# Performance work log

Measured on AMD Instinct MI355X. Metric: run time of the kernel, lower is better.

The kernel has to match this reference:

```python
import jax, jax.numpy as jnp
import numpy as np

D_IN = 1024
D_OUT = 1024


def setup_inputs() -> dict:
    key = jax.random.key(0)
    kx, kq, kk, kv = jax.random.split(key, 4)
    B, S = 4, 2048
    scale = 1.0 / np.sqrt(D_IN)
    return {
        "x": jax.random.normal(kx, (B, S, D_IN), dtype=jnp.float32),
        "Wq": jax.random.normal(kq, (D_IN, D_OUT), dtype=jnp.float32) * scale,
        "Wk": jax.random.normal(kk, (D_IN, D_OUT), dtype=jnp.float32) * scale,
        "Wv": jax.random.normal(kv, (D_IN, D_OUT), dtype=jnp.float32) * scale,
    }


def reference(x, Wq, Wk, Wv):
    # x: [B, S, D_in]; single-head causal attention (dropout=0 -> identity)
    q = jnp.einsum("bsd,de->bse", x, Wq)
    k = jnp.einsum("bsd,de->bse", x, Wk)
    v = jnp.einsum("bsd,de->bse", x, Wv)
    S = x.shape[1]
    d_k = k.shape[-1]
    scores = jnp.einsum("bqe,bke->bqk", q, k) / jnp.sqrt(jnp.float32(d_k))
    causal = jnp.tril(jnp.ones((S, S), dtype=bool))  # True = keep
    scores = jnp.where(causal, scores, -jnp.inf)
    weights = jax.nn.softmax(scores, axis=-1)
    return jnp.einsum("bqk,bke->bqe", weights, v)
```

## Files before the change

### kernel.cpp

```cpp
#include <hip/hip_runtime.h>

typedef unsigned short u16;
typedef __bf16 bf16x8_v __attribute__((ext_vector_type(8)));
typedef float f32x4 __attribute__((ext_vector_type(4)));

__device__ __forceinline__ u16 f2bf(float f) {
    unsigned u = __float_as_uint(f);
    unsigned r = u + 0x7fffu + ((u >> 16) & 1u);
    return (u16)(r >> 16);
}
__device__ __forceinline__ float bf2f(u16 h) {
    return __uint_as_float(((unsigned)h) << 16);
}

__device__ __forceinline__ void gll16(const u16* g, u16* l) {
    __builtin_amdgcn_global_load_lds(
        (const __attribute__((address_space(1))) void*)g,
        (__attribute__((address_space(3))) void*)l, 16, 0, 0);
}

#define EXP_SHIFT 12.0f

__device__ __forceinline__ float* srow_ptr(u16* Sb, int b, int i) {
    return (float*)((char*)Sb + (size_t)b * 8388608 +
                    ((i >> 9) << 12) + 2048 + ((size_t)(i & 511) << 2));
}

__global__ __launch_bounds__(256) void k_prep(const float* __restrict__ x,
                                              const float* __restrict__ Wq,
                                              const float* __restrict__ Wk,
                                              const float* __restrict__ Wv,
                                              u16* __restrict__ xb,
                                              u16* __restrict__ Wt3,
                                              u16* __restrict__ Sb,
                                              float* __restrict__ O) {
    __shared__ float tile[32][33];
    const int bid = blockIdx.x, tid = threadIdx.x;
    if (bid < 4096) {
        int i = (bid * 256 + tid) * 8;
        float4 a = *(const float4*)(x + i);
        float4 bb = *(const float4*)(x + i + 4);
        union { int4 p; u16 h[8]; } o;
        o.h[0] = f2bf(a.x);  o.h[1] = f2bf(a.y);  o.h[2] = f2bf(a.z);  o.h[3] = f2bf(a.w);
        o.h[4] = f2bf(bb.x); o.h[5] = f2bf(bb.y); o.h[6] = f2bf(bb.z); o.h[7] = f2bf(bb.w);
        *(int4*)(xb + i) = o.p;
    } else if (bid < 7168) {
        const int w = bid - 4096;
        const int z = w >> 10, rem = w & 1023;
        const int bx = rem & 31, by = rem >> 5;
        const float* W = (z == 0) ? Wq : (z == 1) ? Wk : Wv;
        u16* Wt = Wt3 + (size_t)z * 1024 * 1024;
        const int tx = tid & 31, ty = tid >> 5;
#pragma unroll
        for (int r = 0; r < 4; ++r)
            tile[ty + r * 8][tx] = W[(by * 32 + ty + r * 8) * 1024 + bx * 32 + tx];
        __syncthreads();
#pragma unroll
        for (int r = 0; r < 4; ++r)
            Wt[(bx * 32 + ty + r * 8) * 1024 + by * 32 + tx] =
                f2bf(tile[tx][ty + r * 8]);
    } else if (bid == 7168) {
        const int chunk = tid >> 7;
        const int t = tid & 127;
        int4 z4 = {0, 0, 0, 0};
#pragma unroll
        for (int c = 0; c < 8; ++c) {
            const int cc = c * 2 + chunk;
            char* p = (char*)Sb + (size_t)(cc >> 2) * 8388608 +
                      ((cc & 3) << 12) + 2048;
            *(int4*)(p + t * 16) = z4;
        }
    } else {
        float4* O4 = (float4*)O;
        const size_t base = (size_t)(bid - 7169) * 1024 + tid;
        float4 z4 = {0.f, 0.f, 0.f, 0.f};
        O4[base] = z4; O4[base + 256] = z4;
        O4[base + 512] = z4; O4[base + 768] = z4;
    }
}

__device__ __forceinline__ void gemm_core_nt(const u16* __restrict__ A,
                                             const u16* __restrict__ B,
                                             int lda, int ldb, int kLen,
                                             u16* smem, f32x4 acc[4][4]) {
    u16* As = smem;
    u16* Bs = smem + 128 * 64;
    const int tid = threadIdx.x;
    const int wave = tid >> 6;
    const int lane = tid & 63;
    const int rowA = tid >> 3;
    const int kcs  = (tid & 7) ^ (rowA & 7);
    const int row16 = lane & 15;
    const int quad = lane >> 4;
    const int sw = row16 & 7;
    const int wm = (wave >> 1) * 64;
    const int wn = (wave & 1) * 64;

#pragma unroll
    for (int i = 0; i < 4; ++i)
#pragma unroll
        for (int j = 0; j < 4; ++j) {
            f32x4 z = {0.f, 0.f, 0.f, 0.f};
            acc[i][j] = z;
        }

    const u16* Ag[4]; const u16* Bg[4];
    u16 *AsB[4], *BsB[4];
#pragma unroll
    for (int u = 0; u < 4; ++u) {
        Ag[u] = A + (size_t)(u * 32 + rowA) * lda + kcs * 8;
        Bg[u] = B + (size_t)(u * 32 + rowA) * ldb + kcs * 8;
        AsB[u] = As + (u * 256 + wave * 64) * 8;
        BsB[u] = Bs + (u * 256 + wave * 64) * 8;
    }

    const int ktiles = kLen >> 6;
    for (int kt = 0; kt < ktiles; ++kt) {
        __syncthreads();
#pragma unroll
        for (int u = 0; u < 4; ++u) gll16(Ag[u] + kt * 64, AsB[u]);
#pragma unroll
        for (int u = 0; u < 4; ++u) gll16(Bg[u] + kt * 64, BsB[u]);
        __syncthreads();
#pragma unroll
        for (int h = 0; h < 2; ++h) {
            bf16x8_v af[4], bfv[4];
            const int cp = (h * 4 + quad);
#pragma unroll
            for (int i = 0; i < 4; ++i)
                af[i] = *(const bf16x8_v*)(As + (wm + i * 16 + row16) * 64 +
                                           (cp ^ sw) * 8);
#pragma unroll
            for (int j = 0; j < 4; ++j)
                bfv[j] = *(const bf16x8_v*)(Bs + (wn + j * 16 + row16) * 64 +
                                            (cp ^ sw) * 8);
#pragma unroll
            for (int i = 0; i < 4; ++i)
#pragma unroll
                for (int j = 0; j < 4; ++j)
                    acc[i][j] = __builtin_amdgcn_mfma_f32_16x16x32_bf16(
                        af[i], bfv[j], acc[i][j], 0, 0, 0);
        }
    }
}

__device__ __forceinline__ void epi_bf16(const f32x4 acc[4][4], u16* smem,
                                         u16* __restrict__ g, int ldg) {
    const int tid = threadIdx.x;
    const int wave = tid >> 6, lane = tid & 63;
    const int row16 = lane & 15, quad = lane >> 4;
    u16* Ts = smem + wave * 2048;
#pragma unroll
    for (int jh = 0; jh < 2; ++jh) {
#pragma unroll
        for (int i = 0; i < 4; ++i)
#pragma unroll
            for (int jj = 0; jj < 2; ++jj) {
                const int j = jh * 2 + jj;
#pragma unroll
                for (int r = 0; r < 4; ++r)
                    Ts[(i * 16 + quad * 4 + r) * 32 + jj * 16 + row16] =
                        f2bf(acc[i][j][r]);
            }
#pragma unroll
        for (int s = 0; s < 4; ++s) {
            const int row = s * 16 + (lane >> 2);
            int4 val = *(const int4*)(Ts + row * 32 + (lane & 3) * 8);
            *(int4*)(g + (size_t)row * ldg + jh * 32 + (lane & 3) * 8) = val;
        }
    }
}

__device__ __forceinline__ void epi_vt(const f32x4 acc[4][4], u16* smem,
                                       u16* __restrict__ Vt, int m0w, int n0w) {
    const int tid = threadIdx.x;
    const int wave = tid >> 6, lane = tid & 63;
    const int row16 = lane & 15, quad = lane >> 4;
    const int b = m0w >> 11;
    const int sBase = m0w & 2047;
    u16* Ts = smem + wave * 4608;
#pragma unroll
    for (int p = 0; p < 2; ++p) {
#pragma unroll
        for (int i = 0; i < 4; ++i)
#pragma unroll
            for (int jj = 0; jj < 2; ++jj) {
                const int j = p * 2 + jj;
                union { unsigned long long d; u16 h[4]; } o;
#pragma unroll
                for (int r = 0; r < 4; ++r) o.h[r] = f2bf(acc[i][j][r]);
                *(unsigned long long*)(Ts + (jj * 16 + row16) * 72 +
                                       i * 16 + quad * 4) = o.d;
            }
#pragma unroll
        for (int rr = 0; rr < 4; ++rr) {
            const int ln = rr * 8 + (lane >> 3);
            const int ck = lane & 7;
            int4 val = *(const int4*)(Ts + ln * 72 + ck * 8);
            const int n = n0w + p * 32 + ln;
            *(int4*)(Vt + ((size_t)b * 1024 + n) * 2048 + sBase + ck * 8) = val;
        }
    }
}

__global__ __launch_bounds__(256, 3) void k_projqk(const u16* __restrict__ X,
                                                   const u16* __restrict__ Wt3,
                                                   u16* __restrict__ Qb,
                                                   u16* __restrict__ Kb) {
    __shared__ u16 smem[16384];
    const int n0g = blockIdx.x * 128, m0 = blockIdx.y * 128;
    f32x4 acc[4][4];
    gemm_core_nt(X + (size_t)m0 * 1024, Wt3 + (size_t)n0g * 1024, 1024, 1024, 1024,
                 smem, acc);
    const int tid = threadIdx.x, wave = tid >> 6;
    const int wm = (wave >> 1) * 64, wn = (wave & 1) * 64;
    __syncthreads();
    u16* Y = (n0g < 1024) ? Qb : Kb;
    const int n0 = n0g & 1023;
    epi_bf16(acc, smem, Y + (size_t)(m0 + wm) * 1024 + n0 + wn, 1024);
}

__global__ __launch_bounds__(256, 3) void k_mix(const u16* __restrict__ X,
                                                const u16* __restrict__ Wt3,
                                                u16* __restrict__ Vt,
                                                const u16* __restrict__ Q,
                                                const u16* __restrict__ Kb,
                                                u16* __restrict__ Sb) {
    __shared__ u16 smem[18432];
    const int bid = blockIdx.x, tid = threadIdx.x;
    const int wave = tid >> 6, lane = tid & 63;
    const int wm = (wave >> 1) * 64, wn = (wave & 1) * 64;
    const int row16 = lane & 15, quad = lane >> 4;

    if (bid < 512) {
        const int nv = bid & 7, m0 = (bid >> 3) * 128;
        f32x4 acc[4][4];
        gemm_core_nt(X + (size_t)m0 * 1024,
                     Wt3 + (size_t)(2048 + nv * 128) * 1024, 1024, 1024, 1024,
                     smem, acc);
        __syncthreads();
        epi_vt(acc, smem, Vt, m0 + wm, nv * 128 + wn);
        return;
    }
    const int lin = bid - 512;
    const int lin2 = (lin & 7) * 68 + (lin >> 3);
    int t = lin2 % 136, b = lin2 / 136;
    int mt = 0;
    while ((mt + 1) * (mt + 2) / 2 <= t) ++mt;
    int nt = t - mt * (mt + 1) / 2;
    const u16* Qp = Q + (size_t)b * 2048 * 1024 + (size_t)mt * 128 * 1024;
    const u16* Kp = Kb + (size_t)b * 2048 * 1024 + (size_t)nt * 128 * 1024;
    u16* Sp = Sb + (size_t)b * 2048 * 2048;
    f32x4 acc[4][4];
    gemm_core_nt(Qp, Kp, 1024, 1024, 1024, smem, acc);
    const int mBase = mt * 128 + wm;
    const int nBase = nt * 128 + wn;
    u16* Ts = smem + wave * 2048;
    float rs[4][4];
#pragma unroll
    for (int i = 0; i < 4; ++i)
#pragma unroll
        for (int r = 0; r < 4; ++r) rs[i][r] = 0.f;

    __syncthreads();
#pragma unroll
    for (int jh = 0; jh < 2; ++jh) {
#pragma unroll
        for (int i = 0; i < 4; ++i)
#pragma unroll
            for (int jj = 0; jj < 2; ++jj) {
                const int j = jh * 2 + jj;
                const int n = nBase + jh * 32 + jj * 16 + row16;
#pragma unroll
                for (int r = 0; r < 4; ++r) {
                    const int m = mBase + i * 16 + quad * 4 + r;
                    float e = 0.f;
                    if (n <= m)
                        e = __expf(acc[i][j][r] * 0.03125f - EXP_SHIFT);
                    rs[i][r] += e;
                    Ts[(i * 16 + quad * 4 + r) * 32 + jj * 16 + row16] = f2bf(e);
                }
            }
#pragma unroll
        for (int s = 0; s < 4; ++s) {
            const int row = s * 16 + (lane >> 2);
            int4 val = *(const int4*)(Ts + row * 32 + (lane & 3) * 8);
            *(int4*)(Sp + (size_t)(mBase + row) * 2048 +
                     nBase + jh * 32 + (lane & 3) * 8) = val;
        }
    }
#pragma unroll
    for (int i = 0; i < 4; ++i)
#pragma unroll
        for (int r = 0; r < 4; ++r) {
            float s = rs[i][r];
#pragma unroll
            for (int off = 1; off < 16; off <<= 1) s += __shfl_xor(s, off);
            if (row16 == 0)
                atomicAdd(srow_ptr((u16*)Sb, b, mBase + i * 16 + quad * 4 + r), s);
        }
}

__global__ __launch_bounds__(256, 4) void k_gemm_pv(u16* __restrict__ P,
                                                    const u16* __restrict__ Vt,
                                                    float* __restrict__ O) {
    __shared__ u16 smem[16384];
    const int bid = blockIdx.x;
    const int c = bid & 7, j = bid >> 3;
    int mt, b, nt, k0, kLen;
    bool split;
    if (j < 32) {
        mt = c; b = j >> 3; nt = j & 7;
        k0 = 0; kLen = (mt + 1) * 128; split = false;
    } else {
        const int q = j - 32;
        mt = 15 - c; b = q >> 4;
        const int r = q & 15;
        nt = r >> 1; kLen = (mt + 1) * 64; k0 = (r & 1) * kLen;
        split = true;
    }
    const u16* Pp = P + (size_t)b * 2048 * 2048 + (size_t)mt * 128 * 2048 + k0;
    const u16* Vp = Vt + (size_t)b * 1024 * 2048 + (size_t)nt * 128 * 2048 + k0;
    f32x4 acc[4][4];
    gemm_core_nt(Pp, Vp, 2048, 2048, kLen, smem, acc);
    float* Op = O + (size_t)b * 2048 * 1024;
    const int tid = threadIdx.x, wave = tid >> 6, lane = tid & 63;
    const int wm = (wave >> 1) * 64, wn = (wave & 1) * 64;
    const int row16 = lane & 15, quad = lane >> 4;
    float inv[4][4];
#pragma unroll
    for (int i = 0; i < 4; ++i)
#pragma unroll
        for (int r = 0; r < 4; ++r)
            inv[i][r] = 1.0f / *srow_ptr(P, b, mt * 128 + wm + i * 16 + quad * 4 + r);
    if (split) {
#pragma unroll
        for (int i = 0; i < 4; ++i)
#pragma unroll
            for (int j2 = 0; j2 < 4; ++j2) {
                int m = mt * 128 + wm + i * 16 + quad * 4;
                int n = nt * 128 + wn + j2 * 16 + row16;
#pragma unroll
                for (int r = 0; r < 4; ++r)
                    unsafeAtomicAdd(&Op[(size_t)(m + r) * 1024 + n],
                                    acc[i][j2][r] * inv[i][r]);
            }
    } else {
#pragma unroll
        for (int i = 0; i < 4; ++i)
#pragma unroll
            for (int j2 = 0; j2 < 4; ++j2) {
                int m = mt * 128 + wm + i * 16 + quad * 4;
                int n = nt * 128 + wn + j2 * 16 + row16;
#pragma unroll
                for (int r = 0; r < 4; ++r)
                    Op[(size_t)(m + r) * 1024 + n] = acc[i][j2][r] * inv[i][r];
            }
    }
}

extern "C" void kernel_launch(void* const* d_in, const int* in_sizes, int n_in,
                              void* d_out, int out_size, void* d_ws, size_t ws_size,
                              hipStream_t stream) {
    const float* x  = (const float*)d_in[0];
    const float* Wq = (const float*)d_in[1];
    const float* Wk = (const float*)d_in[2];
    const float* Wv = (const float*)d_in[3];
    float* out = (float*)d_out;
    char* ws = (char*)d_ws;

    u16* xb  = (u16*)(ws);
    u16* Wt3 = (u16*)(ws + (16u << 20));
    u16* Qb  = (u16*)(ws + (22u << 20));
    u16* Kb  = (u16*)(ws + (38u << 20));
    u16* Vt  = (u16*)(ws + (54u << 20));
    u16* Sb  = (u16*)(ws + (70u << 20));

    k_prep<<<9217, 256, 0, stream>>>(x, Wq, Wk, Wv, xb, Wt3, Sb, out);
    k_projqk<<<dim3(16, 64), 256, 0, stream>>>(xb, Wt3, Qb, Kb);
    k_mix<<<1056, 256, 0, stream>>>(xb, Wt3, Vt, Qb, Kb, Sb);
    k_gemm_pv<<<768, 256, 0, stream>>>(Sb, Vt, out);
}
```

Before: 230.4 us.

## Split V projection from scores kernel and rebalance PV work split by K-chunk

Separates the fused V-projection/scores kernel into two kernels, so the scores GEMM can run with a smaller LDS footprint and a higher occupancy bound. Repartitions the P·V GEMM so each causal row tile splits its K range at 1024, giving blocks more even work. Only the upper half of each batch's output (the rows that need atomics) is zeroed, and the rest is written directly. This trades an extra kernel launch and lost V/scores overlap for better load balance and less zeroing traffic.

```diff
diff --git a/kernel.cpp b/kernel.cpp
--- a/kernel.cpp
+++ b/kernel.cpp
@@ -71,11 +71,15 @@
             *(int4*)(p + t * 16) = z4;
         }
     } else {
-        float4* O4 = (float4*)O;
-        const size_t base = (size_t)(bid - 7169) * 1024 + tid;
+        const int k = bid - 7169;
+        const int b = k >> 8;
+        float* p = O + (size_t)b * 2097152 + 1048576 +
+                   (size_t)(k & 255) * 4096;
         float4 z4 = {0.f, 0.f, 0.f, 0.f};
-        O4[base] = z4; O4[base + 256] = z4;
-        O4[base + 512] = z4; O4[base + 768] = z4;
+        ((float4*)p)[tid]       = z4;
+        ((float4*)p)[tid + 256] = z4;
+        ((float4*)p)[tid + 512] = z4;
+        ((float4*)p)[tid + 768] = z4;
     }
 }
 
@@ -220,29 +224,26 @@
     epi_bf16(acc, smem, Y + (size_t)(m0 + wm) * 1024 + n0 + wn, 1024);
 }
 
-__global__ __launch_bounds__(256, 3) void k_mix(const u16* __restrict__ X,
-                                                const u16* __restrict__ Wt3,
-                                                u16* __restrict__ Vt,
-                                                const u16* __restrict__ Q,
-                                                const u16* __restrict__ Kb,
-                                                u16* __restrict__ Sb) {
+__global__ __launch_bounds__(256, 3) void k_projv(const u16* __restrict__ X,
+                                                  const u16* __restrict__ Wt3,
+                                                  u16* __restrict__ Vt) {
     __shared__ u16 smem[18432];
-    const int bid = blockIdx.x, tid = threadIdx.x;
-    const int wave = tid >> 6, lane = tid & 63;
+    const int nv = blockIdx.x, m0 = blockIdx.y * 128;
+    f32x4 acc[4][4];
+    gemm_core_nt(X + (size_t)m0 * 1024,
+                 Wt3 + (size_t)(2048 + nv * 128) * 1024, 1024, 1024, 1024,
+                 smem, acc);
+    const int tid = threadIdx.x, wave = tid >> 6;
     const int wm = (wave >> 1) * 64, wn = (wave & 1) * 64;
-    const int row16 = lane & 15, quad = lane >> 4;
-
-    if (bid < 512) {
-        const int nv = bid & 7, m0 = (bid >> 3) * 128;
-        f32x4 acc[4][4];
-        gemm_core_nt(X + (size_t)m0 * 1024,
-                     Wt3 + (size_t)(2048 + nv * 128) * 1024, 1024, 1024, 1024,
-                     smem, acc);
-        __syncthreads();
-        epi_vt(acc, smem, Vt, m0 + wm, nv * 128 + wn);
-        return;
-    }
-    const int lin = bid - 512;
+    __syncthreads();
+    epi_vt(acc, smem, Vt, m0 + wm, nv * 128 + wn);
+}
+
+__global__ __launch_bounds__(256, 4) void k_gemm_scores(const u16* __restrict__ Q,
+                                                        const u16* __restrict__ Kb,
+                                                        u16* __restrict__ Sb) {
+    __shared__ u16 smem[16384];
+    const int lin = blockIdx.x;
     const int lin2 = (lin & 7) * 68 + (lin >> 3);
     int t = lin2 % 136, b = lin2 / 136;
     int mt = 0;
@@ -253,6 +254,9 @@
     u16* Sp = Sb + (size_t)b * 2048 * 2048;
     f32x4 acc[4][4];
     gemm_core_nt(Qp, Kp, 1024, 1024, 1024, smem, acc);
+    const int tid = threadIdx.x, wave = tid >> 6, lane = tid & 63;
+    const int wm = (wave >> 1) * 64, wn = (wave & 1) * 64;
+    const int row16 = lane & 15, quad = lane >> 4;
     const int mBase = mt * 128 + wm;
     const int nBase = nt * 128 + wn;
     u16* Ts = smem + wave * 2048;
@@ -306,19 +310,26 @@
                                                     float* __restrict__ O) {
     __shared__ u16 smem[16384];
     const int bid = blockIdx.x;
-    const int c = bid & 7, j = bid >> 3;
-    int mt, b, nt, k0, kLen;
-    bool split;
-    if (j < 32) {
-        mt = c; b = j >> 3; nt = j & 7;
-        k0 = 0; kLen = (mt + 1) * 128; split = false;
-    } else {
-        const int q = j - 32;
-        mt = 15 - c; b = q >> 4;
-        const int r = q & 15;
-        nt = r >> 1; kLen = (mt + 1) * 64; k0 = (r & 1) * kLen;
-        split = true;
-    }
+    const int c = bid & 7;
+    const int slot = bid >> 3;
+    const int nt = slot & 7;
+    const int j = slot >> 3;
+    const int b = j & 3;
+    const int tt = j >> 2;
+    const int t = (tt == 0) ? c : (tt == 1) ? (8 + c) : (22 - (c & 6) + (c & 1));
+    int mt, ch;
+    if (t < 8)       { mt = 15 - t; ch = 0; }
+    else if (t == 8) { mt = 7;      ch = 0; }
+    else if (t == 9) { mt = 15;     ch = 1; }
+    else {
+        const int q = (t - 10) >> 1;
+        if ((t - 10) & 1) { mt = 14 - q; ch = 1; }
+        else              { mt = 6 - q;  ch = 0; }
+    }
+    const int k0 = ch << 10;
+    const int kLen = ch ? (mt - 7) * 128 : ((mt >= 7) ? 1024 : (mt + 1) * 128);
+    const bool full = (ch == 0) && (mt <= 7);
+
     const u16* Pp = P + (size_t)b * 2048 * 2048 + (size_t)mt * 128 * 2048 + k0;
     const u16* Vp = Vt + (size_t)b * 1024 * 2048 + (size_t)nt * 128 * 2048 + k0;
     f32x4 acc[4][4];
@@ -333,7 +344,7 @@
 #pragma unroll
         for (int r = 0; r < 4; ++r)
             inv[i][r] = 1.0f / *srow_ptr(P, b, mt * 128 + wm + i * 16 + quad * 4 + r);
-    if (split) {
+    if (full) {
 #pragma unroll
         for (int i = 0; i < 4; ++i)
 #pragma unroll
@@ -342,8 +353,7 @@
                 int n = nt * 128 + wn + j2 * 16 + row16;
 #pragma unroll
                 for (int r = 0; r < 4; ++r)
-                    unsafeAtomicAdd(&Op[(size_t)(m + r) * 1024 + n],
-                                    acc[i][j2][r] * inv[i][r]);
+                    Op[(size_t)(m + r) * 1024 + n] = acc[i][j2][r] * inv[i][r];
             }
     } else {
 #pragma unroll
@@ -354,7 +364,8 @@
                 int n = nt * 128 + wn + j2 * 16 + row16;
 #pragma unroll
                 for (int r = 0; r < 4; ++r)
-                    Op[(size_t)(m + r) * 1024 + n] = acc[i][j2][r] * inv[i][r];
+                    unsafeAtomicAdd(&Op[(size_t)(m + r) * 1024 + n],
+                                    acc[i][j2][r] * inv[i][r]);
             }
     }
 }
@@ -376,8 +387,9 @@
     u16* Vt  = (u16*)(ws + (54u << 20));
     u16* Sb  = (u16*)(ws + (70u << 20));
 
-    k_prep<<<9217, 256, 0, stream>>>(x, Wq, Wk, Wv, xb, Wt3, Sb, out);
+    k_prep<<<8193, 256, 0, stream>>>(x, Wq, Wk, Wv, xb, Wt3, Sb, out);
     k_projqk<<<dim3(16, 64), 256, 0, stream>>>(xb, Wt3, Qb, Kb);
-    k_mix<<<1056, 256, 0, stream>>>(xb, Wt3, Vt, Qb, Kb, Sb);
+    k_projv<<<dim3(8, 64), 256, 0, stream>>>(xb, Wt3, Vt);
+    k_gemm_scores<<<544, 256, 0, stream>>>(Qb, Kb, Sb);
     k_gemm_pv<<<768, 256, 0, stream>>>(Sb, Vt, out);
 }
```

Result: slower. 235.7 us (+2.3%).
